# Performance work log

Measured on AMD Instinct MI355X. Metric: run time of the kernel, lower is better.

The kernel has to match this reference:

```python
import jax, jax.numpy as jnp
import numpy as np

EPS = 1e-6                                   # VN leaky-relu denominator eps
BN_SCALE = np.float32(1.0 / np.sqrt(1.0 + 1e-5))  # eval-mode BatchNorm with default stats
NEG = 0.2                                    # negative_slope


def vn_lin(x, w):
    # x: [n, c, 3, ...]; w: [c, o] -> [n, o, 3, ...]
    return jnp.einsum('nc...,co->no...', x, w)


def vn_act(p, d):
    # Vector-Neuron leaky ReLU: project p off the half-space defined by direction d.
    dot = jnp.sum(p * d, axis=2, keepdims=True)
    dsq = jnp.sum(d * d, axis=2, keepdims=True)
    corr = p - (dot / (dsq + EPS)) * d
    return NEG * p + (1.0 - NEG) * jnp.where(dot >= 0, p, corr)


def score_net(x, w_vn, wd_vn, w_h1, w_h2, b_h2, temp=1.0):
    # CorrelationNet: VNLinearLeakyReLU(3 -> 2*ks) -> norm -> 1x1 convs -> softmax
    p = vn_lin(x, w_vn) * BN_SCALE           # [N, 2ks, 3, K] (VNBatchNorm ~ scalar in eval)
    d = vn_lin(x, wd_vn)
    s = vn_act(p, d)
    s = jnp.linalg.norm(s, axis=2)           # [N, 2ks, K]
    s = jax.nn.relu(jnp.einsum('nck,co->nok', s, w_h1) * BN_SCALE)  # conv1d k=1, BN, relu
    s = jnp.einsum('nck,co->nok', s, w_h2) + b_h2[None, :, None]     # last conv with bias
    return jax.nn.softmax(s / temp, axis=1)  # [N, ks, K]


def setup_inputs() -> dict:
    key = jax.random.key(0)
    k = [jax.random.fold_in(key, i) for i in range(13)]
    N, N2, K, KS, OUT = 16000, 20000, 16, 8, 64
    half = OUT // 2
    return {
        'q_pts': jax.random.normal(k[0], (N, 3), jnp.float32),
        's_pts': jax.random.normal(k[1], (N2, 3), jnp.float32),
        's_feats': jax.random.normal(k[2], (N2, 1, 3), jnp.float32),
        'neighbor_indices': jax.random.randint(k[3], (N, K), 0, N2),
        'wb': jax.random.normal(k[4], (3, KS * half), jnp.float32) * np.float32(np.sqrt(2.0 / 3.0)),
        'w_vn': jax.random.normal(k[5], (3, 2 * KS), jnp.float32) * 0.5,
        'wd_vn': jax.random.normal(k[6], (3, 2 * KS), jnp.float32) * 0.5,
        'w_h1': jax.random.normal(k[7], (2 * KS, KS), jnp.float32) * 0.25,
        'w_h2': jax.random.normal(k[8], (KS, KS), jnp.float32) * 0.35,
        'b_h2': jnp.zeros((KS,), jnp.float32),
        'wd_relu': jax.random.normal(k[9], (half, half), jnp.float32) * 0.18,
        'w_un': jax.random.normal(k[10], (half, OUT), jnp.float32) * 0.18,
        'wd_un': jax.random.normal(k[11], (half, OUT), jnp.float32) * 0.18,
    }


def reference(q_pts, s_pts, s_feats, neighbor_indices, wb, w_vn, wd_vn,
              w_h1, w_h2, b_h2, wd_relu, w_un, wd_un):
    N, K = neighbor_indices.shape
    KS = w_h2.shape[1]
    # neighbor gather + centering: [N, K, 3] -> [N, 1, 3, K]
    pts = s_pts[neighbor_indices] - q_pts[:, None]
    pts = jnp.transpose(pts, (0, 2, 1))[:, None]
    centers = jnp.broadcast_to(jnp.mean(pts, axis=-1, keepdims=True), pts.shape)
    cross = jnp.cross(pts, centers, axis=2)
    local = jnp.concatenate([pts, centers, cross], axis=1)   # [N, 3, 3, K]
    scores = score_net(local, w_vn, wd_vn, w_h1, w_h2, b_h2)  # [N, KS, K]
    # kernel-point correlation conv
    pro = jnp.einsum('ncdk,cf->nfdk', local, wb)              # [N, KS*half, 3, K]
    pro = pro.reshape(N, KS, -1, 3, K)
    pro = jnp.sum(pro * scores[:, :, None, None, :], axis=1)  # [N, half, 3, K]
    nrm = jnp.linalg.norm(pro, axis=2, keepdims=True)
    normed = pro / jnp.maximum(nrm, 1e-12)                    # F.normalize(p=2, dim=2)
    feats = jnp.mean(normed, axis=-1)                         # [N, half, 3]
    feats = vn_act(feats, vn_lin(feats, wd_relu))             # VNLeakyReLU
    out = vn_act(vn_lin(feats, w_un) * BN_SCALE, vn_lin(feats, wd_un))  # VNLinearLeakyReLU
    return out                                                # [N, out_dim, 3]
```

## Files before the change

kernel.cpp:

```cpp
#include <hip/hip_runtime.h>
#include <math.h>

#define VN_EPS   1e-6f
#define NEG      0.2f
#define POS      0.8f

typedef float v2f __attribute__((ext_vector_type(2)));
typedef float v4f __attribute__((ext_vector_type(4)));

template <int CTRL>
__device__ __forceinline__ float dpp_add(float v) {
    int s = __builtin_amdgcn_update_dpp(0, __float_as_int(v), CTRL, 0xf, 0xf, true);
    return v + __int_as_float(s);
}
__device__ __forceinline__ float row16_allsum(float v) {
    v = dpp_add<0x128>(v);
    v = dpp_add<0x124>(v);
    v = dpp_add<0x122>(v);
    v = dpp_add<0x121>(v);
    return v;
}
__device__ __forceinline__ float row16_sum15(float v) {
    v = dpp_add<0x118>(v);
    v = dpp_add<0x114>(v);
    v = dpp_add<0x112>(v);
    v = dpp_add<0x111>(v);
    return v;
}

__global__ __launch_bounds__(128) void areconv_kernel(
    const float* __restrict__ q_pts,
    const float* __restrict__ s_pts,
    const int*   __restrict__ nbr,
    const float* __restrict__ wb,
    const float* __restrict__ w_vn,
    const float* __restrict__ wd_vn,
    const float* __restrict__ w_h1,
    const float* __restrict__ w_h2,
    const float* __restrict__ b_h2,
    const float* __restrict__ wd_relu,
    const float* __restrict__ w_un,
    const float* __restrict__ wd_un,
    float* __restrict__ out,
    int N)
{
    const float BN_SCALE = 0.999994993f;

    __shared__ __align__(16) float featsA [8][3][36];
    __shared__ __align__(16) float feats2A[8][3][36];

    const int tid  = threadIdx.x;
    const int wv   = tid >> 6;
    const int lane = tid & 63;
    const int p    = lane >> 4;
    const int k    = lane & 15;
    const int bp   = wv * 4 + p;
    int n = blockIdx.x * 8 + bp;
    n = (n < N) ? n : (N - 1);

    const float qx = q_pts[n * 3 + 0];
    const float qy = q_pts[n * 3 + 1];
    const float qz = q_pts[n * 3 + 2];
    const int   id = nbr[n * 16 + k];
    const float px = s_pts[id * 3 + 0] - qx;
    const float py = s_pts[id * 3 + 1] - qy;
    const float pz = s_pts[id * 3 + 2] - qz;

    const float cx = row16_allsum(px) * 0.0625f;
    const float cy = row16_allsum(py) * 0.0625f;
    const float cz = row16_allsum(pz) * 0.0625f;

    const float rx = py * cz - pz * cy;
    const float ry = pz * cx - px * cz;
    const float rz = px * cy - py * cx;

    const float L[3][3] = {{px, py, pz}, {cx, cy, cz}, {rx, ry, rz}};

    v2f t01 = {0.f, 0.f}, t23 = t01, t45 = t01, t67 = t01;
#pragma unroll 1
    for (int o = 0; o < 16; ++o) {
        const float wv0 = w_vn[o],  wv1 = w_vn[16 + o],  wv2 = w_vn[32 + o];
        const float wd0 = wd_vn[o], wd1 = wd_vn[16 + o], wd2 = wd_vn[32 + o];
        float pv[3], dv[3];
        float dot = 0.f, dsq = 0.f;
#pragma unroll
        for (int d = 0; d < 3; ++d) {
            const float pp = BN_SCALE * (L[0][d] * wv0 + L[1][d] * wv1 + L[2][d] * wv2);
            const float dd = L[0][d] * wd0 + L[1][d] * wd1 + L[2][d] * wd2;
            pv[d] = pp; dv[d] = dd;
            dot += pp * dd;
            dsq += dd * dd;
        }
        const float f = dot * __builtin_amdgcn_rcpf(dsq + VN_EPS);
        float acc = 0.f;
#pragma unroll
        for (int d = 0; d < 3; ++d) {
            const float corr = pv[d] - f * dv[d];
            const float sel  = (dot >= 0.f) ? pv[d] : corr;
            const float a    = NEG * pv[d] + POS * sel;
            acc += a * a;
        }
        const float s = __builtin_amdgcn_sqrtf(acc);
        t01 += s * (*(const v2f*)&w_h1[o * 8 + 0]);
        t23 += s * (*(const v2f*)&w_h1[o * 8 + 2]);
        t45 += s * (*(const v2f*)&w_h1[o * 8 + 4]);
        t67 += s * (*(const v2f*)&w_h1[o * 8 + 6]);
    }
    float tt[8];
    tt[0] = fmaxf(t01[0] * BN_SCALE, 0.f);  tt[1] = fmaxf(t01[1] * BN_SCALE, 0.f);
    tt[2] = fmaxf(t23[0] * BN_SCALE, 0.f);  tt[3] = fmaxf(t23[1] * BN_SCALE, 0.f);
    tt[4] = fmaxf(t45[0] * BN_SCALE, 0.f);  tt[5] = fmaxf(t45[1] * BN_SCALE, 0.f);
    tt[6] = fmaxf(t67[0] * BN_SCALE, 0.f);  tt[7] = fmaxf(t67[1] * BN_SCALE, 0.f);

    float sc[8];
    float mx = -1e30f;
#pragma unroll
    for (int op = 0; op < 4; ++op) {
        v2f u = *(const v2f*)&b_h2[2 * op];
#pragma unroll
        for (int c = 0; c < 8; ++c)
            u += tt[c] * (*(const v2f*)&w_h2[c * 8 + 2 * op]);
        sc[2 * op + 0] = u[0];
        sc[2 * op + 1] = u[1];
        mx = fmaxf(mx, fmaxf(u[0], u[1]));
    }
    float se = 0.f;
#pragma unroll
    for (int o = 0; o < 8; ++o) { sc[o] = __expf(sc[o] - mx); se += sc[o]; }
    const float inv_se = __builtin_amdgcn_rcpf(se);
#pragma unroll
    for (int o = 0; o < 8; ++o) sc[o] *= inv_se;

#pragma unroll 1
    for (int grp = 0; grp < 8; ++grp) {
        const int hb = grp * 4;
        v4f W0 = sc[0] * (*(const v4f*)&wb[0 * 256 + hb]);
        v4f W1 = sc[0] * (*(const v4f*)&wb[1 * 256 + hb]);
        v4f W2 = sc[0] * (*(const v4f*)&wb[2 * 256 + hb]);
#pragma unroll
        for (int s = 1; s < 8; ++s) {
            const float sv = sc[s];
            W0 += sv * (*(const v4f*)&wb[0 * 256 + s * 32 + hb]);
            W1 += sv * (*(const v4f*)&wb[1 * 256 + s * 32 + hb]);
            W2 += sv * (*(const v4f*)&wb[2 * 256 + s * 32 + hb]);
        }
        v4f V0 = L[0][0] * W0 + L[1][0] * W1 + L[2][0] * W2;
        v4f V1 = L[0][1] * W0 + L[1][1] * W1 + L[2][1] * W2;
        v4f V2 = L[0][2] * W0 + L[1][2] * W1 + L[2][2] * W2;
        v4f vv = V0 * V0 + V1 * V1 + V2 * V2;
        v4f inn;
#pragma unroll
        for (int e = 0; e < 4; ++e)
            inn[e] = __builtin_amdgcn_rsqf(fmaxf(vv[e], 1e-24f)) * 0.0625f;
        V0 *= inn; V1 *= inn; V2 *= inn;
        v4f X0, X1, X2;
#pragma unroll
        for (int e = 0; e < 4; ++e) {
            X0[e] = row16_sum15(V0[e]);
            X1[e] = row16_sum15(V1[e]);
            X2[e] = row16_sum15(V2[e]);
        }
        if (k == 15) {
            *(v4f*)&featsA[bp][0][hb] = X0;
            *(v4f*)&featsA[bp][1][hb] = X1;
            *(v4f*)&featsA[bp][2][hb] = X2;
        }
    }

    {
        v2f D0 = {0.f, 0.f}, D1 = D0, D2 = D0;
#pragma unroll 1
        for (int grp = 0; grp < 8; ++grp) {
            const int hb = grp * 4;
            const v4f f0 = *(const v4f*)&featsA[bp][0][hb];
            const v4f f1 = *(const v4f*)&featsA[bp][1][hb];
            const v4f f2 = *(const v4f*)&featsA[bp][2][hb];
#pragma unroll
            for (int e = 0; e < 4; ++e) {
                const v2f w = *(const v2f*)&wd_relu[(hb + e) * 32 + 2 * k];
                D0 += f0[e] * w;
                D1 += f1[e] * w;
                D2 += f2[e] * w;
            }
        }
        v2f R0, R1, R2;
#pragma unroll
        for (int j = 0; j < 2; ++j) {
            const int o = 2 * k + j;
            const float p0 = featsA[bp][0][o];
            const float p1 = featsA[bp][1][o];
            const float p2 = featsA[bp][2][o];
            const float d0 = D0[j], d1 = D1[j], d2 = D2[j];
            const float dot = p0 * d0 + p1 * d1 + p2 * d2;
            const float dsq = d0 * d0 + d1 * d1 + d2 * d2;
            const float f   = dot * __builtin_amdgcn_rcpf(dsq + VN_EPS);
            const bool  pos = (dot >= 0.f);
            R0[j] = NEG * p0 + POS * (pos ? p0 : (p0 - f * d0));
            R1[j] = NEG * p1 + POS * (pos ? p1 : (p1 - f * d1));
            R2[j] = NEG * p2 + POS * (pos ? p2 : (p2 - f * d2));
        }
        *(v2f*)&feats2A[bp][0][2 * k] = R0;
        *(v2f*)&feats2A[bp][1][2 * k] = R1;
        *(v2f*)&feats2A[bp][2][2 * k] = R2;
    }

    {
        v4f AU0 = (v4f)0.f, AU1 = AU0, AU2 = AU0;
        v4f AV0 = AU0, AV1 = AU0, AV2 = AU0;
#pragma unroll 1
        for (int grp = 0; grp < 8; ++grp) {
            const int hb = grp * 4;
            const v4f f0 = *(const v4f*)&feats2A[bp][0][hb];
            const v4f f1 = *(const v4f*)&feats2A[bp][1][hb];
            const v4f f2 = *(const v4f*)&feats2A[bp][2][hb];
#pragma unroll
            for (int e = 0; e < 4; ++e) {
                const v4f wu = *(const v4f*)&w_un [(hb + e) * 64 + 4 * k];
                const v4f wd = *(const v4f*)&wd_un[(hb + e) * 64 + 4 * k];
                AU0 += f0[e] * wu; AU1 += f1[e] * wu; AU2 += f2[e] * wu;
                AV0 += f0[e] * wd; AV1 += f1[e] * wd; AV2 += f2[e] * wd;
            }
        }
        float O[12];
#pragma unroll
        for (int e = 0; e < 4; ++e) {
            const float u0 = AU0[e] * BN_SCALE;
            const float u1 = AU1[e] * BN_SCALE;
            const float u2 = AU2[e] * BN_SCALE;
            const float v0 = AV0[e], v1 = AV1[e], v2 = AV2[e];
            const float dot = u0 * v0 + u1 * v1 + u2 * v2;
            const float dsq = v0 * v0 + v1 * v1 + v2 * v2;
            const float f   = dot * __builtin_amdgcn_rcpf(dsq + VN_EPS);
            const bool  pos = (dot >= 0.f);
            O[3 * e + 0] = NEG * u0 + POS * (pos ? u0 : (u0 - f * v0));
            O[3 * e + 1] = NEG * u1 + POS * (pos ? u1 : (u1 - f * v1));
            O[3 * e + 2] = NEG * u2 + POS * (pos ? u2 : (u2 - f * v2));
        }
        float* dst = out + (long)n * 192 + 12 * k;
        *(v4f*)(dst + 0) = *(const v4f*)&O[0];
        *(v4f*)(dst + 4) = *(const v4f*)&O[4];
        *(v4f*)(dst + 8) = *(const v4f*)&O[8];
    }
}

extern "C" void kernel_launch(void* const* d_in, const int* in_sizes, int n_in,
                              void* d_out, int out_size, void* d_ws, size_t ws_size,
                              hipStream_t stream) {
    const float* q_pts   = (const float*)d_in[0];
    const float* s_pts   = (const float*)d_in[1];
    const int*   nbr     = (const int*)  d_in[3];
    const float* wb      = (const float*)d_in[4];
    const float* w_vn    = (const float*)d_in[5];
    const float* wd_vn   = (const float*)d_in[6];
    const float* w_h1    = (const float*)d_in[7];
    const float* w_h2    = (const float*)d_in[8];
    const float* b_h2    = (const float*)d_in[9];
    const float* wd_relu = (const float*)d_in[10];
    const float* w_un    = (const float*)d_in[11];
    const float* wd_un   = (const float*)d_in[12];
    float* out = (float*)d_out;

    const int N = in_sizes[0] / 3;
    const int blocks = (N + 7) / 8;
    areconv_kernel<<<blocks, 128, 0, stream>>>(
        q_pts, s_pts, nbr, wb, w_vn, wd_vn, w_h1, w_h2, b_h2,
        wd_relu, w_un, wd_un, out, N);
}
```

Before: 107.7 us.

## Split each point across two 16-lane groups to double thread parallelism

Each point is now handled by 32 lanes instead of 16. Two half-groups each redundantly compute the neighbour geometry and scores, then split the 32 half-channels of the correlation conv and the output channels between them. Blocks grow to 256 threads while still covering 8 points, and per-lane register and accumulator use shrinks (v4f to v2f) so occupancy can rise under launch_bounds(256,8). The cost is duplicated score-net work per point and narrower vector loads and stores. No barrier is added between the featsA writes and the cross-half reads, even though both half-groups sit in the same wavefront.

```diff
diff --git a/kernel.cpp b/kernel.cpp
--- a/kernel.cpp
+++ b/kernel.cpp
@@ -28,7 +28,7 @@
     return v;
 }
 
-__global__ __launch_bounds__(128) void areconv_kernel(
+__global__ __launch_bounds__(256, 8) void areconv_kernel(
     const float* __restrict__ q_pts,
     const float* __restrict__ s_pts,
     const int*   __restrict__ nbr,
@@ -52,10 +52,12 @@
     const int tid  = threadIdx.x;
     const int wv   = tid >> 6;
     const int lane = tid & 63;
-    const int p    = lane >> 4;
+    const int half = lane >> 5;
+    const int p    = (lane >> 4) & 1;
     const int k    = lane & 15;
-    const int bp   = wv * 4 + p;
-    int n = blockIdx.x * 8 + bp;
+    const int pt   = wv * 2 + p;
+    const int lwp  = half * 16 + k;
+    int n = blockIdx.x * 8 + pt;
     n = (n < N) ? n : (N - 1);
 
     const float qx = q_pts[n * 3 + 0];
@@ -132,8 +134,8 @@
     for (int o = 0; o < 8; ++o) sc[o] *= inv_se;
 
 #pragma unroll 1
-    for (int grp = 0; grp < 8; ++grp) {
-        const int hb = grp * 4;
+    for (int grp = 0; grp < 4; ++grp) {
+        const int hb = half * 16 + grp * 4;
         v4f W0 = sc[0] * (*(const v4f*)&wb[0 * 256 + hb]);
         v4f W1 = sc[0] * (*(const v4f*)&wb[1 * 256 + hb]);
         v4f W2 = sc[0] * (*(const v4f*)&wb[2 * 256 + hb]);
@@ -161,85 +163,77 @@
             X2[e] = row16_sum15(V2[e]);
         }
         if (k == 15) {
-            *(v4f*)&featsA[bp][0][hb] = X0;
-            *(v4f*)&featsA[bp][1][hb] = X1;
-            *(v4f*)&featsA[bp][2][hb] = X2;
+            *(v4f*)&featsA[pt][0][hb] = X0;
+            *(v4f*)&featsA[pt][1][hb] = X1;
+            *(v4f*)&featsA[pt][2][hb] = X2;
         }
     }
 
     {
-        v2f D0 = {0.f, 0.f}, D1 = D0, D2 = D0;
+        const int o = lwp;
+        float D0 = 0.f, D1 = 0.f, D2 = 0.f;
 #pragma unroll 1
         for (int grp = 0; grp < 8; ++grp) {
             const int hb = grp * 4;
-            const v4f f0 = *(const v4f*)&featsA[bp][0][hb];
-            const v4f f1 = *(const v4f*)&featsA[bp][1][hb];
-            const v4f f2 = *(const v4f*)&featsA[bp][2][hb];
+            const v4f f0 = *(const v4f*)&featsA[pt][0][hb];
+            const v4f f1 = *(const v4f*)&featsA[pt][1][hb];
+            const v4f f2 = *(const v4f*)&featsA[pt][2][hb];
 #pragma unroll
             for (int e = 0; e < 4; ++e) {
-                const v2f w = *(const v2f*)&wd_relu[(hb + e) * 32 + 2 * k];
+                const float w = wd_relu[(hb + e) * 32 + o];
                 D0 += f0[e] * w;
                 D1 += f1[e] * w;
                 D2 += f2[e] * w;
             }
         }
-        v2f R0, R1, R2;
-#pragma unroll
-        for (int j = 0; j < 2; ++j) {
-            const int o = 2 * k + j;
-            const float p0 = featsA[bp][0][o];
-            const float p1 = featsA[bp][1][o];
-            const float p2 = featsA[bp][2][o];
-            const float d0 = D0[j], d1 = D1[j], d2 = D2[j];
-            const float dot = p0 * d0 + p1 * d1 + p2 * d2;
-            const float dsq = d0 * d0 + d1 * d1 + d2 * d2;
-            const float f   = dot * __builtin_amdgcn_rcpf(dsq + VN_EPS);
-            const bool  pos = (dot >= 0.f);
-            R0[j] = NEG * p0 + POS * (pos ? p0 : (p0 - f * d0));
-            R1[j] = NEG * p1 + POS * (pos ? p1 : (p1 - f * d1));
-            R2[j] = NEG * p2 + POS * (pos ? p2 : (p2 - f * d2));
-        }
-        *(v2f*)&feats2A[bp][0][2 * k] = R0;
-        *(v2f*)&feats2A[bp][1][2 * k] = R1;
-        *(v2f*)&feats2A[bp][2][2 * k] = R2;
+        const float p0 = featsA[pt][0][o];
+        const float p1 = featsA[pt][1][o];
+        const float p2 = featsA[pt][2][o];
+        const float dot = p0 * D0 + p1 * D1 + p2 * D2;
+        const float dsq = D0 * D0 + D1 * D1 + D2 * D2;
+        const float f   = dot * __builtin_amdgcn_rcpf(dsq + VN_EPS);
+        const bool  pos = (dot >= 0.f);
+        feats2A[pt][0][o] = NEG * p0 + POS * (pos ? p0 : (p0 - f * D0));
+        feats2A[pt][1][o] = NEG * p1 + POS * (pos ? p1 : (p1 - f * D1));
+        feats2A[pt][2][o] = NEG * p2 + POS * (pos ? p2 : (p2 - f * D2));
     }
 
     {
-        v4f AU0 = (v4f)0.f, AU1 = AU0, AU2 = AU0;
-        v4f AV0 = AU0, AV1 = AU0, AV2 = AU0;
+        v2f AU0 = {0.f, 0.f}, AU1 = AU0, AU2 = AU0;
+        v2f AV0 = AU0, AV1 = AU0, AV2 = AU0;
 #pragma unroll 1
         for (int grp = 0; grp < 8; ++grp) {
             const int hb = grp * 4;
-            const v4f f0 = *(const v4f*)&feats2A[bp][0][hb];
-            const v4f f1 = *(const v4f*)&feats2A[bp][1][hb];
-            const v4f f2 = *(const v4f*)&feats2A[bp][2][hb];
+            const v4f f0 = *(const v4f*)&feats2A[pt][0][hb];
+            const v4f f1 = *(const v4f*)&feats2A[pt][1][hb];
+            const v4f f2 = *(const v4f*)&feats2A[pt][2][hb];
 #pragma unroll
             for (int e = 0; e < 4; ++e) {
-                const v4f wu = *(const v4f*)&w_un [(hb + e) * 64 + 4 * k];
-                const v4f wd = *(const v4f*)&wd_un[(hb + e) * 64 + 4 * k];
+                const v2f wu = *(const v2f*)&w_un [(hb + e) * 64 + 2 * lwp];
+                const v2f wd = *(const v2f*)&wd_un[(hb + e) * 64 + 2 * lwp];
                 AU0 += f0[e] * wu; AU1 += f1[e] * wu; AU2 += f2[e] * wu;
                 AV0 += f0[e] * wd; AV1 += f1[e] * wd; AV2 += f2[e] * wd;
             }
         }
-        float O[12];
-#pragma unroll
-        for (int e = 0; e < 4; ++e) {
-            const float u0 = AU0[e] * BN_SCALE;
-            const float u1 = AU1[e] * BN_SCALE;
-            const float u2 = AU2[e] * BN_SCALE;
-            const float v0 = AV0[e], v1 = AV1[e], v2 = AV2[e];
+        float O[6];
+#pragma unroll
+        for (int j = 0; j < 2; ++j) {
+            const float u0 = AU0[j] * BN_SCALE;
+            const float u1 = AU1[j] * BN_SCALE;
+            const float u2 = AU2[j] * BN_SCALE;
+            const float v0 = AV0[j], v1 = AV1[j], v2 = AV2[j];
             const float dot = u0 * v0 + u1 * v1 + u2 * v2;
             const float dsq = v0 * v0 + v1 * v1 + v2 * v2;
             const float f   = dot * __builtin_amdgcn_rcpf(dsq + VN_EPS);
             const bool  pos = (dot >= 0.f);
-            O[3 * e + 0] = NEG * u0 + POS * (pos ? u0 : (u0 - f * v0));
-            O[3 * e + 1] = NEG * u1 + POS * (pos ? u1 : (u1 - f * v1));
-            O[3 * e + 2] = NEG * u2 + POS * (pos ? u2 : (u2 - f * v2));
-        }
-        float* dst = out + (long)n * 192 + 12 * k;
-        *(v4f*)(dst + 0) = *(const v4f*)&O[0];
-        *(v4f*)(dst + 4) = *(const v4f*)&O[4];
-        *(v4f*)(dst + 8) = *(const v4f*)&O[8];
+            O[3 * j + 0] = NEG * u0 + POS * (pos ? u0 : (u0 - f * v0));
+            O[3 * j + 1] = NEG * u1 + POS * (pos ? u1 : (u1 - f * v1));
+            O[3 * j + 2] = NEG * u2 + POS * (pos ? u2 : (u2 - f * v2));
+        }
+        float* dst = out + (long)n * 192 + 6 * lwp;
+        *(v2f*)(dst + 0) = *(const v2f*)&O[0];
+        *(v2f*)(dst + 2) = *(const v2f*)&O[2];
+        *(v2f*)(dst + 4) = *(const v2f*)&O[4];
     }
 }
 
@@ -262,7 +256,7 @@
 
     const int N = in_sizes[0] / 3;
     const int blocks = (N + 7) / 8;
-    areconv_kernel<<<blocks, 128, 0, stream>>>(
+    areconv_kernel<<<blocks, 256, 0, stream>>>(
         q_pts, s_pts, nbr, wb, w_vn, wd_vn, w_h1, w_h2, b_h2,
         wd_relu, w_un, wd_un, out, N);
 }
```

New measurement: 174.7 us. 62.2% more time.
